# Kernel tuning notes

Measured on AMD Instinct MI355X. Metric: run time of the kernel, lower is better.

Reference implementation:

```python
import jax, jax.numpy as jnp
import numpy as np

G, N, E = 16, 512, 2048        # graphs, nodes/graph, edges/graph
CN, CE = 64, 64                # node / edge feature channels
K = 3                          # Laguerre polynomial order
RATIO = 0.5
KEEP = int(np.ceil(RATIO * N)) # 256 kept nodes per graph (static)
POWER_ITERS = 64               # power iteration approximating eigsh(k=1,'LM')


def setup_inputs() -> dict:
    key = jax.random.key(0)
    ks = jax.random.split(key, 10)
    x_n = jax.random.normal(ks[0], (G * N, CN), jnp.float32)
    x_e = jax.random.normal(ks[1], (G * E, CE), jnp.float32)
    # incidence endpoints per edge, local node ids, no self loops
    u = jax.random.randint(ks[2], (G, E), 0, N)
    v = (u + 1 + jax.random.randint(ks[3], (G, E), 0, N - 1)) % N
    # node-level conv graph (global ids within per-graph blocks): both directions
    offs = (jnp.arange(G) * N)[:, None]
    src_n = jnp.concatenate([(u + offs).reshape(-1), (v + offs).reshape(-1)])
    dst_n = jnp.concatenate([(v + offs).reshape(-1), (u + offs).reshape(-1)])
    edge_weight_n = jax.random.uniform(ks[4], (src_n.shape[0],), jnp.float32)
    # edge-level conv graph (global ids within per-graph edge blocks)
    ME = 4 * E
    offs_e = (jnp.arange(G) * E)[:, None]
    src_e = (jax.random.randint(ks[5], (G, ME), 0, E) + offs_e).reshape(-1)
    dst_e = (jax.random.randint(ks[6], (G, ME), 0, E) + offs_e).reshape(-1)
    edge_weight_e = jax.random.uniform(ks[7], (src_e.shape[0],), jnp.float32)
    # HodgeLaguerreConv(C -> 1, K) weights (glorot-ish) + bias (zeros init)
    W_n = jax.random.normal(ks[8], (K, CN), jnp.float32) / np.sqrt(CN)
    b_n = jnp.zeros((1,), jnp.float32)
    W_e = jax.random.normal(ks[9], (K, CE), jnp.float32) / np.sqrt(CE)
    b_e = jnp.zeros((1,), jnp.float32)
    return dict(x_n=x_n, x_e=x_e, edge_u=u, edge_v=v,
                src_n=src_n, dst_n=dst_n, edge_weight_n=edge_weight_n,
                src_e=src_e, dst_e=dst_e, edge_weight_e=edge_weight_e,
                W_n=W_n, b_n=b_n, W_e=W_e, b_e=b_e)


def hodge_laguerre(x, src, dst, w, Wk, b):
    """HodgeLaguerreConv with out_channels=1: out = sum_k T_k(L) x @ Wk[k] + b.
    T_0 = x; T_1 = x - Lx; T_{k+1} = (-L T_k + (2k+1) T_k - k T_{k-1})/(k+1)."""
    num = x.shape[0]
    def L(z):  # scatter-add message passing: out[i] = sum_{j->i} norm * z[j]
        return jax.ops.segment_sum(w[:, None] * z[src], dst, num_segments=num)
    Tx0 = x
    out = Tx0 @ Wk[0]
    Tx1 = x - L(x)
    out = out + Tx1 @ Wk[1]
    k = 1
    for i in range(2, Wk.shape[0]):
        Tx2 = (-L(Tx1) + (2 * k + 1) * Tx1 - k * Tx0) / (k + 1)
        out = out + Tx2 @ Wk[i]
        Tx0, Tx1 = Tx1, Tx2
        k += 1
    return out + b[0]


def pool_graph(sn, se, xn, xe, u, v):
    # node score augmented by |B1| @ edge_score (abs incidence gathers both endpoints)
    aug = sn.at[u].add(se).at[v].add(se)
    perm = jnp.argsort(-aug)                    # descending sort, take top KEEP
    mask_n = jnp.zeros((N,), xn.dtype).at[perm[:KEEP]].set(1.0)
    # mask_e = |B1|^T (1 - mask_n); keep edge iff both endpoints kept (== 0)
    bad = (1.0 - mask_n[u]) + (1.0 - mask_n[v])
    keep_e = (bad == 0.0).astype(xn.dtype)
    # dense incidence B1 [N, E]: -1 at source row, +1 at target row
    cols = jnp.arange(E)
    B = jnp.zeros((N, E), xn.dtype).at[u, cols].add(-1.0).at[v, cols].add(1.0)
    Bm = B * mask_n[:, None] * keep_e[None, :]  # row/col masking (zero-padded)
    L0 = Bm @ Bm.T                              # [N, N] node Laplacian
    L1 = Bm.T @ Bm                              # [E, E] edge Laplacian
    # power iteration for lambda_max(L0) (== eigsh k=1 'LM'; zero rows keep spectrum)
    w = jnp.ones((N,), xn.dtype) / np.sqrt(N)
    for _ in range(POWER_ITERS):
        w = L0 @ w
        w = w / (jnp.linalg.norm(w) + 1e-12)
    lam = w @ (L0 @ w)
    scale = 2.0 / (lam + 1e-12)
    return xn * mask_n[:, None], L0 * scale, xe * keep_e[:, None], L1 * scale


def reference(x_n, x_e, edge_u, edge_v, src_n, dst_n, edge_weight_n,
              src_e, dst_e, edge_weight_e, W_n, b_n, W_e, b_e):
    score_n = jax.nn.sigmoid(hodge_laguerre(x_n, src_n, dst_n, edge_weight_n, W_n, b_n).reshape(-1))
    score_e = jax.nn.sigmoid(hodge_laguerre(x_e, src_e, dst_e, edge_weight_e, W_e, b_e).reshape(-1))
    xn_g = (x_n * score_n[:, None]).reshape(G, N, CN)
    xe_g = (x_e * score_e[:, None]).reshape(G, E, CE)
    sn = score_n.reshape(G, N)
    se = score_e.reshape(G, E)
    return jax.vmap(pool_graph)(sn, se, xn_g, xe_g, edge_u, edge_v)
```

## Files before the change

### kernel.cpp

```cpp
#include <hip/hip_runtime.h>
#include <math.h>

#define GG 16
#define NNODE 512
#define EEDGE 2048
#define KEEPN 256
#define PITERS 64
#define NNT 8192
#define NET 32768

#define WS_C1N 0
#define WS_C2N 8192
#define WS_BN  16384
#define WS_SN  24576
#define WS_C1E 32768
#define WS_C2E 65536
#define WS_BE  98304
#define WS_SE  131072
#define WS_MASK 163840
#define WS_KEEP 172032
#define WS_KLIST 204800
#define WS_KCNT 237568
#define WS_SCALE 237584

#define O_XN 0
#define O_L0 524288
#define O_XE 4718592
#define O_L1 6815744

#define L04 1048576
#define ZTOT4 17825792
#define ZB1 7340032
#define ZB2 14680064

__device__ __forceinline__ void zero_range(float* __restrict__ out, int lo, int hi,
                                           int start, int stride) {
  float4 z = make_float4(0.f, 0.f, 0.f, 0.f);
  float4* o4 = (float4*)out;
  for (int i = lo + start; i < hi; i += stride) {
    int f = (i < L04) ? (O_L0 / 4 + i) : (O_L1 / 4 + (i - L04));
    o4[f] = z;
  }
}

__global__ __launch_bounds__(256) void k_dots(const float* __restrict__ xn,
    const float* __restrict__ xe, const float* __restrict__ Wn,
    const float* __restrict__ We, float* __restrict__ ws, float* __restrict__ out) {
  if (blockIdx.x >= 10240) {
    zero_range(out, 0, ZB1, (blockIdx.x - 10240) * 256 + threadIdx.x, 262144);
    return;
  }
  int gw = (blockIdx.x * 256 + threadIdx.x) >> 6;
  int lane = threadIdx.x & 63;
  const float* x; const float* W; int row; float *c1, *c2, *bs;
  if (gw < NNT) {
    row = gw; x = xn + (size_t)row * 64; W = Wn;
    c1 = ws + WS_C1N; c2 = ws + WS_C2N; bs = ws + WS_BN;
  } else {
    row = gw - NNT;
    x = xe + (size_t)row * 64; W = We;
    c1 = ws + WS_C1E; c2 = ws + WS_C2E; bs = ws + WS_BE;
  }
  float v = x[lane];
  float r0 = v * W[lane];
  float r1 = v * W[64 + lane];
  float r2 = v * W[128 + lane];
  for (int o = 32; o; o >>= 1) {
    r0 += __shfl_xor(r0, o, 64);
    r1 += __shfl_xor(r1, o, 64);
    r2 += __shfl_xor(r2, o, 64);
  }
  if (lane == 0) { c1[row] = r1; c2[row] = r2; bs[row] = r0 + r1 + r2; }
}

__global__ __launch_bounds__(256) void k_msg(
    const int* __restrict__ src_n, const int* __restrict__ dst_n, const float* __restrict__ wn,
    const int* __restrict__ src_e, const int* __restrict__ dst_e, const float* __restrict__ we,
    const float* __restrict__ bnp, const float* __restrict__ bep,
    float* __restrict__ ws, float* __restrict__ out) {
  if (blockIdx.x >= 32) {
    zero_range(out, ZB1, ZB2, (blockIdx.x - 32) * 256 + threadIdx.x, 262144);
    return;
  }
  __shared__ float sm[5 * 2048];
  float* c1 = sm;
  float* c2 = sm + 2048;
  float* d1 = sm + 4096;
  float* d2 = sm + 6144;
  float* e2 = sm + 8192;
  const int tid = threadIdx.x;
  const bool isNode = blockIdx.x < 16;
  const int g = isNode ? blockIdx.x : blockIdx.x - 16;
  const int n = isNode ? NNODE : EEDGE;
  const int roff = g * n;
  const float* C1 = ws + (isNode ? WS_C1N : WS_C1E) + roff;
  const float* C2 = ws + (isNode ? WS_C2N : WS_C2E) + roff;
  const float* BB = ws + (isNode ? WS_BN : WS_BE) + roff;
  float* S = ws + (isNode ? WS_SN : WS_SE) + roff;
  const float bias = isNode ? bnp[0] : bep[0];
  const int ecnt = isNode ? 4096 : 8192;
  const int* SA = isNode ? src_n : src_e;
  const int* DA = isNode ? dst_n : dst_e;
  const float* WA = isNode ? wn : we;

  for (int i = tid; i < n; i += 256) {
    c1[i] = C1[i]; c2[i] = C2[i]; d1[i] = 0.f; d2[i] = 0.f; e2[i] = 0.f;
  }
  __syncthreads();
  for (int t = tid; t < ecnt; t += 256) {
    int idx = isNode ? ((t < 2048) ? g * 2048 + t : 32768 + g * 2048 + (t - 2048))
                     : g * 8192 + t;
    int s = SA[idx] - roff, d = DA[idx] - roff;
    float w = WA[idx];
    atomicAdd(&d1[d], w * c1[s]);
    atomicAdd(&d2[d], w * c2[s]);
  }
  __syncthreads();
  for (int t = tid; t < ecnt; t += 256) {
    int idx = isNode ? ((t < 2048) ? g * 2048 + t : 32768 + g * 2048 + (t - 2048))
                     : g * 8192 + t;
    int s = SA[idx] - roff, d = DA[idx] - roff;
    float w = WA[idx];
    atomicAdd(&e2[d], w * d2[s]);
  }
  __syncthreads();
  for (int i = tid; i < n; i += 256) {
    float t = BB[i] - d1[i] - 2.0f * d2[i] + 0.5f * e2[i] + bias;
    S[i] = 1.0f / (1.0f + expf(-t));
  }
}

__global__ __launch_bounds__(512) void k_pool(
    const int* __restrict__ edge_u, const int* __restrict__ edge_v,
    float* __restrict__ ws, float* __restrict__ out) {
  const int tid = threadIdx.x;
  if (blockIdx.x >= 16) {
    zero_range(out, ZB2, ZTOT4, (blockIdx.x - 16) * 512 + tid, 262144);
    return;
  }
  const int g = blockIdx.x;
  __shared__ float aug[NNODE];
  __shared__ float key[NNODE];
  __shared__ int kidx[NNODE];
  __shared__ int su[EEDGE];
  __shared__ int sv[EEDGE];
  __shared__ int maskS[NNODE];
  __shared__ int degS[NNODE];
  __shared__ int offS[NNODE];
  __shared__ int adj[2 * EEDGE];
  __shared__ float wv[NNODE];
  __shared__ float red[8];
  __shared__ int kcnt;
  int* wsi = (int*)ws;

  int nidx = g * NNODE + tid;
  aug[tid] = ws[WS_SN + nidx];
  for (int e = tid; e < EEDGE; e += 512) {
    su[e] = edge_u[g * EEDGE + e];
    sv[e] = edge_v[g * EEDGE + e];
  }
  if (tid == 0) kcnt = 0;
  maskS[tid] = 0;
  __syncthreads();
  for (int e = tid; e < EEDGE; e += 512) {
    float s = ws[WS_SE + g * EEDGE + e];
    atomicAdd(&aug[su[e]], s);
    atomicAdd(&aug[sv[e]], s);
  }
  __syncthreads();
  key[tid] = aug[tid]; kidx[tid] = tid;
  __syncthreads();
  for (int k = 2; k <= NNODE; k <<= 1) {
    for (int j = k >> 1; j > 0; j >>= 1) {
      int i = tid, ixj = i ^ j;
      if (ixj > i) {
        float ka = key[i], kb = key[ixj];
        int ia = kidx[i], ib = kidx[ixj];
        bool aAfter = (ka < kb) || (ka == kb && ia > ib);
        bool doswap = ((i & k) == 0) ? aAfter : !aAfter;
        if (doswap) { key[i] = kb; key[ixj] = ka; kidx[i] = ib; kidx[ixj] = ia; }
      }
      __syncthreads();
    }
  }
  if (tid < KEEPN) maskS[kidx[tid]] = 1;
  degS[tid] = 0;
  __syncthreads();
  wsi[WS_MASK + nidx] = maskS[tid];
  for (int e = tid; e < EEDGE; e += 512) {
    int k = maskS[su[e]] & maskS[sv[e]];
    wsi[WS_KEEP + g * EEDGE + e] = k;
    if (k) {
      int p = atomicAdd(&kcnt, 1);
      wsi[WS_KLIST + g * EEDGE + p] = e;
      atomicAdd(&degS[su[e]], 1);
      atomicAdd(&degS[sv[e]], 1);
    }
  }
  __syncthreads();
  if (tid == 0) wsi[WS_KCNT + g] = kcnt;
  int* t0 = (int*)key;
  t0[tid] = degS[tid];
  __syncthreads();
  for (int s = 1; s < NNODE; s <<= 1) {
    int v = t0[tid] + ((tid >= s) ? t0[tid - s] : 0);
    __syncthreads();
    t0[tid] = v;
    __syncthreads();
  }
  offS[tid] = t0[tid] - degS[tid];
  __syncthreads();
  for (int e = tid; e < EEDGE; e += 512) {
    if (maskS[su[e]] & maskS[sv[e]]) {
      int pu = atomicAdd(&offS[su[e]], 1); adj[pu] = sv[e];
      int pv = atomicAdd(&offS[sv[e]], 1); adj[pv] = su[e];
    }
  }
  __syncthreads();
  int myDeg = degS[tid];
  int myEnd = offS[tid];
  int myStart = myEnd - myDeg;
  const int lane = tid & 63;
  const int wvid = tid >> 6;
  wv[tid] = 0.04419417382415922f;
  __syncthreads();
  for (int it = 0; it < PITERS; ++it) {
    float acc = (float)myDeg * wv[tid];
    for (int p = myStart; p < myEnd; ++p) acc -= wv[adj[p]];
    float sq = acc * acc;
    for (int o = 32; o; o >>= 1) sq += __shfl_xor(sq, o, 64);
    if (lane == 0) red[wvid] = sq;
    __syncthreads();
    float tot = red[0] + red[1] + red[2] + red[3] + red[4] + red[5] + red[6] + red[7];
    float rn = 1.0f / (sqrtf(tot) + 1e-12f);
    wv[tid] = acc * rn;
    __syncthreads();
  }
  {
    float acc = (float)myDeg * wv[tid];
    for (int p = myStart; p < myEnd; ++p) acc -= wv[adj[p]];
    float pr = wv[tid] * acc;
    for (int o = 32; o; o >>= 1) pr += __shfl_xor(pr, o, 64);
    if (lane == 0) red[wvid] = pr;
    __syncthreads();
    if (tid == 0) {
      float lam = red[0] + red[1] + red[2] + red[3] + red[4] + red[5] + red[6] + red[7];
      ws[WS_SCALE + g] = 2.0f / (lam + 1e-12f);
    }
  }
}

__global__ __launch_bounds__(256) void k_out(
    const float* __restrict__ xn, const float* __restrict__ xe,
    const int* __restrict__ edge_u, const int* __restrict__ edge_v,
    const float* __restrict__ ws, float* __restrict__ out) {
  int b = blockIdx.x, tid = threadIdx.x;
  const int* wsi = (const int*)ws;
  if (b < 512) {
    int idx = b * 256 + tid;
    int row = idx >> 4;
    float s = ws[WS_SN + row] * (float)wsi[WS_MASK + row];
    float4 x4 = ((const float4*)xn)[idx];
    ((float4*)(out + O_XN))[idx] = make_float4(x4.x * s, x4.y * s, x4.z * s, x4.w * s);
  } else if (b < 2560) {
    int idx = (b - 512) * 256 + tid;
    int row = idx >> 4;
    float s = ws[WS_SE + row] * (float)wsi[WS_KEEP + row];
    float4 x4 = ((const float4*)xe)[idx];
    ((float4*)(out + O_XE))[idx] = make_float4(x4.x * s, x4.y * s, x4.z * s, x4.w * s);
  } else if (b < 2576) {
    int g = b - 2560;
    int cnt = wsi[WS_KCNT + g];
    float s = ws[WS_SCALE + g];
    float* L0 = out + O_L0 + (long long)g * (NNODE * NNODE);
    const int* kl = wsi + WS_KLIST + g * EEDGE;
    const int* eu = edge_u + g * EEDGE;
    const int* ev = edge_v + g * EEDGE;
    for (int t = tid; t < cnt; t += 256) {
      int e = kl[t];
      int u = eu[e], v = ev[e];
      atomicAdd(&L0[u * NNODE + u], s);
      atomicAdd(&L0[v * NNODE + v], s);
      atomicAdd(&L0[u * NNODE + v], -s);
      atomicAdd(&L0[v * NNODE + u], -s);
    }
  } else {
    int q = b - 2576;
    int g = q >> 8, sb = q & 255;
    int cnt = wsi[WS_KCNT + g];
    float s = ws[WS_SCALE + g];
    float* L1 = out + O_L1 + (long long)g * (EEDGE * EEDGE);
    const int* kl = wsi + WS_KLIST + g * EEDGE;
    const int* eu = edge_u + g * EEDGE;
    const int* ev = edge_v + g * EEDGE;
    for (int a = sb; a < cnt; a += 256) {
      int e1 = kl[a];
      int u1 = eu[e1], v1 = ev[e1];
      long long rowoff = (long long)e1 * EEDGE;
      for (int b2 = tid; b2 < cnt; b2 += 256) {
        int e2 = kl[b2];
        int u2 = eu[e2], v2 = ev[e2];
        int val = (u1 == u2) + (v1 == v2) - (v1 == u2) - (u1 == v2);
        if (val) L1[rowoff + e2] = s * (float)val;
      }
    }
  }
}

extern "C" void kernel_launch(void* const* d_in, const int* in_sizes, int n_in,
                              void* d_out, int out_size, void* d_ws, size_t ws_size,
                              hipStream_t stream) {
  const float* x_n = (const float*)d_in[0];
  const float* x_e = (const float*)d_in[1];
  const int* edge_u = (const int*)d_in[2];
  const int* edge_v = (const int*)d_in[3];
  const int* src_n = (const int*)d_in[4];
  const int* dst_n = (const int*)d_in[5];
  const float* ew_n = (const float*)d_in[6];
  const int* src_e = (const int*)d_in[7];
  const int* dst_e = (const int*)d_in[8];
  const float* ew_e = (const float*)d_in[9];
  const float* W_n = (const float*)d_in[10];
  const float* b_n = (const float*)d_in[11];
  const float* W_e = (const float*)d_in[12];
  const float* b_e = (const float*)d_in[13];
  float* ws = (float*)d_ws;
  float* out = (float*)d_out;

  k_dots<<<10240 + 1024, 256, 0, stream>>>(x_n, x_e, W_n, W_e, ws, out);
  k_msg<<<32 + 1024, 256, 0, stream>>>(src_n, dst_n, ew_n, src_e, dst_e, ew_e,
                                       b_n, b_e, ws, out);
  k_pool<<<16 + 512, 512, 0, stream>>>(edge_u, edge_v, ws, out);
  k_out<<<6672, 256, 0, stream>>>(x_n, x_e, edge_u, edge_v, ws, out);
}
```

Baseline: 513.2 us.

## Fuse message passing into pool kernel, replace sort with rank count, lazy normalization

Moves the per-graph Laguerre message passing into the pooling kernel so scores stay in shared memory, and merges all output zeroing into that kernel. It replaces the bitonic sort with a direct rank count, the shared-memory scan with a wave-shuffle scan, and normalizes the power iterate only every eighth step using double buffers. The aim is fewer launches and barriers. In exchange, 16 blocks now carry more serial work, and lazy normalization risks larger intermediate magnitudes.

After: 481.7 us. 6.1% less time.

```diff
diff --git a/kernel.cpp b/kernel.cpp
--- a/kernel.cpp
+++ b/kernel.cpp
@@ -12,16 +12,14 @@
 #define WS_C1N 0
 #define WS_C2N 8192
 #define WS_BN  16384
-#define WS_SN  24576
-#define WS_C1E 32768
-#define WS_C2E 65536
-#define WS_BE  98304
-#define WS_SE  131072
-#define WS_MASK 163840
-#define WS_KEEP 172032
-#define WS_KLIST 204800
-#define WS_KCNT 237568
-#define WS_SCALE 237584
+#define WS_C1E 24576
+#define WS_C2E 57344
+#define WS_BE  90112
+#define WS_SNW 122880
+#define WS_SEW 131072
+#define WS_KLIST 163840
+#define WS_KCNT 196608
+#define WS_SCALE 196624
 
 #define O_XN 0
 #define O_L0 524288
@@ -30,26 +28,10 @@
 
 #define L04 1048576
 #define ZTOT4 17825792
-#define ZB1 7340032
-#define ZB2 14680064
-
-__device__ __forceinline__ void zero_range(float* __restrict__ out, int lo, int hi,
-                                           int start, int stride) {
-  float4 z = make_float4(0.f, 0.f, 0.f, 0.f);
-  float4* o4 = (float4*)out;
-  for (int i = lo + start; i < hi; i += stride) {
-    int f = (i < L04) ? (O_L0 / 4 + i) : (O_L1 / 4 + (i - L04));
-    o4[f] = z;
-  }
-}
 
 __global__ __launch_bounds__(256) void k_dots(const float* __restrict__ xn,
     const float* __restrict__ xe, const float* __restrict__ Wn,
-    const float* __restrict__ We, float* __restrict__ ws, float* __restrict__ out) {
-  if (blockIdx.x >= 10240) {
-    zero_range(out, 0, ZB1, (blockIdx.x - 10240) * 256 + threadIdx.x, 262144);
-    return;
-  }
+    const float* __restrict__ We, float* __restrict__ ws) {
   int gw = (blockIdx.x * 256 + threadIdx.x) >> 6;
   int lane = threadIdx.x & 63;
   const float* x; const float* W; int row; float *c1, *c2, *bs;
@@ -73,178 +55,197 @@
   if (lane == 0) { c1[row] = r1; c2[row] = r2; bs[row] = r0 + r1 + r2; }
 }
 
-__global__ __launch_bounds__(256) void k_msg(
+#define SB 3104
+__global__ __launch_bounds__(512) void k_pool(
     const int* __restrict__ src_n, const int* __restrict__ dst_n, const float* __restrict__ wn,
     const int* __restrict__ src_e, const int* __restrict__ dst_e, const float* __restrict__ we,
+    const int* __restrict__ edge_u, const int* __restrict__ edge_v,
     const float* __restrict__ bnp, const float* __restrict__ bep,
-    float* __restrict__ ws, float* __restrict__ out) {
-  if (blockIdx.x >= 32) {
-    zero_range(out, ZB1, ZB2, (blockIdx.x - 32) * 256 + threadIdx.x, 262144);
-    return;
-  }
-  __shared__ float sm[5 * 2048];
-  float* c1 = sm;
-  float* c2 = sm + 2048;
-  float* d1 = sm + 4096;
-  float* d2 = sm + 6144;
-  float* e2 = sm + 8192;
-  const int tid = threadIdx.x;
-  const bool isNode = blockIdx.x < 16;
-  const int g = isNode ? blockIdx.x : blockIdx.x - 16;
-  const int n = isNode ? NNODE : EEDGE;
-  const int roff = g * n;
-  const float* C1 = ws + (isNode ? WS_C1N : WS_C1E) + roff;
-  const float* C2 = ws + (isNode ? WS_C2N : WS_C2E) + roff;
-  const float* BB = ws + (isNode ? WS_BN : WS_BE) + roff;
-  float* S = ws + (isNode ? WS_SN : WS_SE) + roff;
-  const float bias = isNode ? bnp[0] : bep[0];
-  const int ecnt = isNode ? 4096 : 8192;
-  const int* SA = isNode ? src_n : src_e;
-  const int* DA = isNode ? dst_n : dst_e;
-  const float* WA = isNode ? wn : we;
-
-  for (int i = tid; i < n; i += 256) {
-    c1[i] = C1[i]; c2[i] = C2[i]; d1[i] = 0.f; d2[i] = 0.f; e2[i] = 0.f;
-  }
-  __syncthreads();
-  for (int t = tid; t < ecnt; t += 256) {
-    int idx = isNode ? ((t < 2048) ? g * 2048 + t : 32768 + g * 2048 + (t - 2048))
-                     : g * 8192 + t;
-    int s = SA[idx] - roff, d = DA[idx] - roff;
-    float w = WA[idx];
-    atomicAdd(&d1[d], w * c1[s]);
-    atomicAdd(&d2[d], w * c2[s]);
-  }
-  __syncthreads();
-  for (int t = tid; t < ecnt; t += 256) {
-    int idx = isNode ? ((t < 2048) ? g * 2048 + t : 32768 + g * 2048 + (t - 2048))
-                     : g * 8192 + t;
-    int s = SA[idx] - roff, d = DA[idx] - roff;
-    float w = WA[idx];
-    atomicAdd(&e2[d], w * d2[s]);
-  }
-  __syncthreads();
-  for (int i = tid; i < n; i += 256) {
-    float t = BB[i] - d1[i] - 2.0f * d2[i] + 0.5f * e2[i] + bias;
-    S[i] = 1.0f / (1.0f + expf(-t));
-  }
-}
-
-__global__ __launch_bounds__(512) void k_pool(
-    const int* __restrict__ edge_u, const int* __restrict__ edge_v,
     float* __restrict__ ws, float* __restrict__ out) {
   const int tid = threadIdx.x;
   if (blockIdx.x >= 16) {
-    zero_range(out, ZB2, ZTOT4, (blockIdx.x - 16) * 512 + tid, 262144);
+    float4 z = make_float4(0.f, 0.f, 0.f, 0.f);
+    float4* o4 = (float4*)out;
+    int start = (blockIdx.x - 16) * 512 + tid;
+    for (int i = start; i < ZTOT4; i += 2048 * 512) {
+      int f = (i < L04) ? (O_L0 / 4 + i) : (O_L1 / 4 + (i - L04));
+      o4[f] = z;
+    }
     return;
   }
+  __shared__ float smem[13856];
+  int* smi = (int*)smem;
+  float* seS = smem;
+  float* aug = smem + 2048;
+  float* snw = smem + 2560;
+  float* red = smem + 3072;
+  int*   iws = smi + 3080;
+  int*   kcp = smi + 3088;
+  float* c1n = smem + SB;        float* c2n = smem + SB + 512;
+  float* d1n = smem + SB + 1024; float* d2n = smem + SB + 1536;
+  float* e2n = smem + SB + 2048;
+  float* c1e = smem + SB;        float* c2e = smem + SB + 2048;
+  float* d1e = smem + SB + 4096; float* d2e = smem + SB + 6144;
+  float* e2e = smem + SB + 8192;
+  int* suL  = smi + SB;          int* svL  = smi + SB + 2048;
+  int* maskS = smi + SB + 4096;  int* degS = smi + SB + 4608;
+  int* offS = smi + SB + 5120;   int* adj  = smi + SB + 5632;
+  float* wvA = smem + SB + 9728; float* wvB = smem + SB + 10240;
+
   const int g = blockIdx.x;
-  __shared__ float aug[NNODE];
-  __shared__ float key[NNODE];
-  __shared__ int kidx[NNODE];
-  __shared__ int su[EEDGE];
-  __shared__ int sv[EEDGE];
-  __shared__ int maskS[NNODE];
-  __shared__ int degS[NNODE];
-  __shared__ int offS[NNODE];
-  __shared__ int adj[2 * EEDGE];
-  __shared__ float wv[NNODE];
-  __shared__ float red[8];
-  __shared__ int kcnt;
+  const int roffN = g * NNODE;
+  const int roffE = g * EEDGE;
+  const int lane = tid & 63, wid = tid >> 6;
+
+  if (tid < NNODE) {
+    c1n[tid] = ws[WS_C1N + roffN + tid];
+    c2n[tid] = ws[WS_C2N + roffN + tid];
+    d1n[tid] = 0.f; d2n[tid] = 0.f; e2n[tid] = 0.f;
+  }
+  __syncthreads();
+  for (int t = tid; t < 4096; t += 512) {
+    int idx = (t < 2048) ? (g * 2048 + t) : (32768 + g * 2048 + (t - 2048));
+    int s = src_n[idx] - roffN, d = dst_n[idx] - roffN;
+    float w = wn[idx];
+    atomicAdd(&d1n[d], w * c1n[s]);
+    atomicAdd(&d2n[d], w * c2n[s]);
+  }
+  __syncthreads();
+  for (int t = tid; t < 4096; t += 512) {
+    int idx = (t < 2048) ? (g * 2048 + t) : (32768 + g * 2048 + (t - 2048));
+    int s = src_n[idx] - roffN, d = dst_n[idx] - roffN;
+    atomicAdd(&e2n[d], wn[idx] * d2n[s]);
+  }
+  __syncthreads();
+  float biasN = bnp[0], biasE = bep[0];
+  if (tid < NNODE) {
+    float t = ws[WS_BN + roffN + tid] - d1n[tid] - 2.0f * d2n[tid]
+            + 0.5f * e2n[tid] + biasN;
+    float s = 1.0f / (1.0f + expf(-t));
+    snw[tid] = s; aug[tid] = s;
+  }
+  __syncthreads();
+
+  for (int i = tid; i < EEDGE; i += 512) {
+    c1e[i] = ws[WS_C1E + roffE + i];
+    c2e[i] = ws[WS_C2E + roffE + i];
+    d1e[i] = 0.f; d2e[i] = 0.f; e2e[i] = 0.f;
+  }
+  __syncthreads();
+  for (int t = tid; t < 8192; t += 512) {
+    int idx = g * 8192 + t;
+    int s = src_e[idx] - roffE, d = dst_e[idx] - roffE;
+    float w = we[idx];
+    atomicAdd(&d1e[d], w * c1e[s]);
+    atomicAdd(&d2e[d], w * c2e[s]);
+  }
+  __syncthreads();
+  for (int t = tid; t < 8192; t += 512) {
+    int idx = g * 8192 + t;
+    int s = src_e[idx] - roffE, d = dst_e[idx] - roffE;
+    atomicAdd(&e2e[d], we[idx] * d2e[s]);
+  }
+  __syncthreads();
+  for (int e = tid; e < EEDGE; e += 512) {
+    float t = ws[WS_BE + roffE + e] - d1e[e] - 2.0f * d2e[e]
+            + 0.5f * e2e[e] + biasE;
+    float s = 1.0f / (1.0f + expf(-t));
+    seS[e] = s;
+    atomicAdd(&aug[edge_u[roffE + e]], s);
+    atomicAdd(&aug[edge_v[roffE + e]], s);
+  }
+  __syncthreads();
+
+  {
+    float a = aug[tid];
+    int r = 0;
+    #pragma unroll 8
+    for (int j = 0; j < NNODE; ++j) {
+      float b = aug[j];
+      r += (b > a) || (b == a && j < tid);
+    }
+    maskS[tid] = (r < KEEPN) ? 1 : 0;
+    degS[tid] = 0;
+  }
+  for (int e = tid; e < EEDGE; e += 512) {
+    suL[e] = edge_u[roffE + e];
+    svL[e] = edge_v[roffE + e];
+  }
+  if (tid == 0) *kcp = 0;
+  __syncthreads();
+  ws[WS_SNW + roffN + tid] = snw[tid] * (float)maskS[tid];
+
   int* wsi = (int*)ws;
-
-  int nidx = g * NNODE + tid;
-  aug[tid] = ws[WS_SN + nidx];
   for (int e = tid; e < EEDGE; e += 512) {
-    su[e] = edge_u[g * EEDGE + e];
-    sv[e] = edge_v[g * EEDGE + e];
-  }
-  if (tid == 0) kcnt = 0;
-  maskS[tid] = 0;
-  __syncthreads();
+    int u = suL[e], v = svL[e];
+    int k = maskS[u] & maskS[v];
+    ws[WS_SEW + roffE + e] = seS[e] * (float)k;
+    if (k) {
+      int p = atomicAdd(kcp, 1);
+      wsi[WS_KLIST + roffE + p] = e;
+      atomicAdd(&degS[u], 1);
+      atomicAdd(&degS[v], 1);
+    }
+  }
+  __syncthreads();
+  if (tid == 0) wsi[WS_KCNT + g] = *kcp;
+
+  int dv = degS[tid];
+  int inc = dv;
+  for (int o = 1; o < 64; o <<= 1) {
+    int t = __shfl_up(inc, o, 64);
+    if (lane >= o) inc += t;
+  }
+  if (lane == 63) iws[wid] = inc;
+  __syncthreads();
+  int base = 0;
+  for (int k = 0; k < wid; ++k) base += iws[k];
+  int myStart = base + inc - dv;
+  offS[tid] = myStart;
+  __syncthreads();
+
   for (int e = tid; e < EEDGE; e += 512) {
-    float s = ws[WS_SE + g * EEDGE + e];
-    atomicAdd(&aug[su[e]], s);
-    atomicAdd(&aug[sv[e]], s);
-  }
-  __syncthreads();
-  key[tid] = aug[tid]; kidx[tid] = tid;
-  __syncthreads();
-  for (int k = 2; k <= NNODE; k <<= 1) {
-    for (int j = k >> 1; j > 0; j >>= 1) {
-      int i = tid, ixj = i ^ j;
-      if (ixj > i) {
-        float ka = key[i], kb = key[ixj];
-        int ia = kidx[i], ib = kidx[ixj];
-        bool aAfter = (ka < kb) || (ka == kb && ia > ib);
-        bool doswap = ((i & k) == 0) ? aAfter : !aAfter;
-        if (doswap) { key[i] = kb; key[ixj] = ka; kidx[i] = ib; kidx[ixj] = ia; }
-      }
+    int u = suL[e], v = svL[e];
+    if (maskS[u] & maskS[v]) {
+      int pu = atomicAdd(&offS[u], 1); adj[pu] = v;
+      int pv = atomicAdd(&offS[v], 1); adj[pv] = u;
+    }
+  }
+  __syncthreads();
+  int myDeg = dv;
+  int myEnd = offS[tid];
+
+  wvA[tid] = 0.04419417382415922f;
+  __syncthreads();
+  float* wcur = wvA; float* wnext = wvB;
+  for (int it = 0; it < PITERS; ++it) {
+    float acc = (float)myDeg * wcur[tid];
+    for (int p = myStart; p < myEnd; ++p) acc -= wcur[adj[p]];
+    if ((it & 7) == 7) {
+      float sq = acc * acc;
+      for (int o = 32; o; o >>= 1) sq += __shfl_xor(sq, o, 64);
+      if (lane == 0) red[wid] = sq;
       __syncthreads();
-    }
-  }
-  if (tid < KEEPN) maskS[kidx[tid]] = 1;
-  degS[tid] = 0;
-  __syncthreads();
-  wsi[WS_MASK + nidx] = maskS[tid];
-  for (int e = tid; e < EEDGE; e += 512) {
-    int k = maskS[su[e]] & maskS[sv[e]];
-    wsi[WS_KEEP + g * EEDGE + e] = k;
-    if (k) {
-      int p = atomicAdd(&kcnt, 1);
-      wsi[WS_KLIST + g * EEDGE + p] = e;
-      atomicAdd(&degS[su[e]], 1);
-      atomicAdd(&degS[sv[e]], 1);
-    }
-  }
-  __syncthreads();
-  if (tid == 0) wsi[WS_KCNT + g] = kcnt;
-  int* t0 = (int*)key;
-  t0[tid] = degS[tid];
-  __syncthreads();
-  for (int s = 1; s < NNODE; s <<= 1) {
-    int v = t0[tid] + ((tid >= s) ? t0[tid - s] : 0);
+      float tot = red[0] + red[1] + red[2] + red[3]
+                + red[4] + red[5] + red[6] + red[7];
+      wnext[tid] = acc * (1.0f / (sqrtf(tot) + 1e-12f));
+    } else {
+      wnext[tid] = acc;
+    }
     __syncthreads();
-    t0[tid] = v;
-    __syncthreads();
-  }
-  offS[tid] = t0[tid] - degS[tid];
-  __syncthreads();
-  for (int e = tid; e < EEDGE; e += 512) {
-    if (maskS[su[e]] & maskS[sv[e]]) {
-      int pu = atomicAdd(&offS[su[e]], 1); adj[pu] = sv[e];
-      int pv = atomicAdd(&offS[sv[e]], 1); adj[pv] = su[e];
-    }
-  }
-  __syncthreads();
-  int myDeg = degS[tid];
-  int myEnd = offS[tid];
-  int myStart = myEnd - myDeg;
-  const int lane = tid & 63;
-  const int wvid = tid >> 6;
-  wv[tid] = 0.04419417382415922f;
-  __syncthreads();
-  for (int it = 0; it < PITERS; ++it) {
-    float acc = (float)myDeg * wv[tid];
-    for (int p = myStart; p < myEnd; ++p) acc -= wv[adj[p]];
-    float sq = acc * acc;
-    for (int o = 32; o; o >>= 1) sq += __shfl_xor(sq, o, 64);
-    if (lane == 0) red[wvid] = sq;
-    __syncthreads();
-    float tot = red[0] + red[1] + red[2] + red[3] + red[4] + red[5] + red[6] + red[7];
-    float rn = 1.0f / (sqrtf(tot) + 1e-12f);
-    wv[tid] = acc * rn;
-    __syncthreads();
+    float* tmp = wcur; wcur = wnext; wnext = tmp;
   }
   {
-    float acc = (float)myDeg * wv[tid];
-    for (int p = myStart; p < myEnd; ++p) acc -= wv[adj[p]];
-    float pr = wv[tid] * acc;
+    float wv_ = wcur[tid];
+    float acc = (float)myDeg * wv_;
+    for (int p = myStart; p < myEnd; ++p) acc -= wcur[adj[p]];
+    float pr = wv_ * acc;
     for (int o = 32; o; o >>= 1) pr += __shfl_xor(pr, o, 64);
-    if (lane == 0) red[wvid] = pr;
+    if (lane == 0) red[wid] = pr;
     __syncthreads();
     if (tid == 0) {
-      float lam = red[0] + red[1] + red[2] + red[3] + red[4] + red[5] + red[6] + red[7];
+      float lam = red[0] + red[1] + red[2] + red[3]
+                + red[4] + red[5] + red[6] + red[7];
       ws[WS_SCALE + g] = 2.0f / (lam + 1e-12f);
     }
   }
@@ -259,13 +260,13 @@
   if (b < 512) {
     int idx = b * 256 + tid;
     int row = idx >> 4;
-    float s = ws[WS_SN + row] * (float)wsi[WS_MASK + row];
+    float s = ws[WS_SNW + row];
     float4 x4 = ((const float4*)xn)[idx];
     ((float4*)(out + O_XN))[idx] = make_float4(x4.x * s, x4.y * s, x4.z * s, x4.w * s);
   } else if (b < 2560) {
     int idx = (b - 512) * 256 + tid;
     int row = idx >> 4;
-    float s = ws[WS_SE + row] * (float)wsi[WS_KEEP + row];
+    float s = ws[WS_SEW + row];
     float4 x4 = ((const float4*)xe)[idx];
     ((float4*)(out + O_XE))[idx] = make_float4(x4.x * s, x4.y * s, x4.z * s, x4.w * s);
   } else if (b < 2576) {
@@ -327,9 +328,8 @@
   float* ws = (float*)d_ws;
   float* out = (float*)d_out;
 
-  k_dots<<<10240 + 1024, 256, 0, stream>>>(x_n, x_e, W_n, W_e, ws, out);
-  k_msg<<<32 + 1024, 256, 0, stream>>>(src_n, dst_n, ew_n, src_e, dst_e, ew_e,
-                                       b_n, b_e, ws, out);
-  k_pool<<<16 + 512, 512, 0, stream>>>(edge_u, edge_v, ws, out);
+  k_dots<<<10240, 256, 0, stream>>>(x_n, x_e, W_n, W_e, ws);
+  k_pool<<<16 + 2048, 512, 0, stream>>>(src_n, dst_n, ew_n, src_e, dst_e, ew_e,
+                                        edge_u, edge_v, b_n, b_e, ws, out);
   k_out<<<6672, 256, 0, stream>>>(x_n, x_e, edge_u, edge_v, ws, out);
 }
```
